# Kernel optimization log

Hardware: AMD Instinct MI355X
Metric: run time of the kernel (lower is better)

The kernel has to match this reference:

```python
import jax, jax.numpy as jnp
import numpy as np

B, S, D, H = 2, 2048, 1024, 16
DK = D // H  # 64


def rotate_half(x):
    d = x.shape[-1]
    x1, x2 = x[..., : d // 2], x[..., d // 2 :]
    return jnp.concatenate([-x2, x1], axis=-1)


def apply_rope(q, k):
    # q, k: [B, H, S, DK]
    d_k = q.shape[-1]
    seq_len = q.shape[-2]
    theta = 10000.0 ** (-2.0 / d_k * jnp.arange(d_k // 2, dtype=q.dtype))
    positions = jnp.arange(seq_len, dtype=q.dtype)
    angles = jnp.outer(positions, theta)                    # [S, DK/2]
    cos = jnp.tile(jnp.cos(angles), (1, 2))                 # [S, DK]
    sin = jnp.tile(jnp.sin(angles), (1, 2))
    q = q * cos + rotate_half(q) * sin
    k = k * cos + rotate_half(k) * sin
    return q, k


def setup_inputs() -> dict:
    key = jax.random.key(0)
    ks = jax.random.split(key, 9)
    std = 1.0 / np.sqrt(D)
    x = jax.random.normal(ks[0], (B, S, D), dtype=jnp.float32)
    # mask True = masked (code uses masked_fill(mask, -inf)); causal mask
    mask = jnp.triu(jnp.ones((S, S), dtype=bool), k=1)[None, None, :, :]
    mask = jnp.broadcast_to(mask, (B, 1, S, S))
    Wq = jax.random.uniform(ks[1], (D, D), jnp.float32, -std, std)
    bq = jax.random.uniform(ks[2], (D,), jnp.float32, -std, std)
    Wk = jax.random.uniform(ks[3], (D, D), jnp.float32, -std, std)
    bk = jax.random.uniform(ks[4], (D,), jnp.float32, -std, std)
    Wv = jax.random.uniform(ks[5], (D, D), jnp.float32, -std, std)
    bv = jax.random.uniform(ks[6], (D,), jnp.float32, -std, std)
    Wo = jax.random.uniform(ks[7], (D, D), jnp.float32, -std, std)
    bo = jax.random.uniform(ks[8], (D,), jnp.float32, -std, std)
    return {"x": x, "mask": mask, "Wq": Wq, "bq": bq, "Wk": Wk, "bk": bk,
            "Wv": Wv, "bv": bv, "Wo": Wo, "bo": bo}


def reference(x, mask, Wq, bq, Wk, bk, Wv, bv, Wo, bo):
    b, s, d = x.shape
    # projections -> [B, H, S, DK]
    q = (x @ Wq + bq).reshape(b, s, H, DK).transpose(0, 2, 1, 3)
    k = (x @ Wk + bk).reshape(b, s, H, DK).transpose(0, 2, 1, 3)
    v = (x @ Wv + bv).reshape(b, s, H, DK).transpose(0, 2, 1, 3)
    q, k = apply_rope(q, k)
    scores = jnp.einsum("bhqd,bhkd->bhqk", q, k) / np.sqrt(DK)
    scores = jnp.where(mask, -jnp.inf, scores)
    probs = jax.nn.softmax(scores, axis=-1)
    attn = jnp.einsum("bhqk,bhkd->bhqd", probs, v)
    o = attn.transpose(0, 2, 1, 3).reshape(b, s, H * DK)
    return o @ Wo + bo
```

## Files before the change

### kernel.cpp

```cpp
#include <hip/hip_runtime.h>
#include <hip/hip_bf16.h>
#include <math.h>

typedef __hip_bfloat16 bf16;
typedef __attribute__((ext_vector_type(8))) short short8;
typedef __attribute__((ext_vector_type(4))) short s16x4;
typedef __attribute__((ext_vector_type(4))) float f32x4;

#define B_  2
#define S_  2048
#define D_  1024
#define H_  16
#define DK_ 64

#define QSCALE 0.18033688011112043f
#define EXPOFF 11.541560327111707f

__device__ inline short bfs(float f) { return __builtin_bit_cast(short, __float2bfloat16(f)); }

#define GLL16(gptr, lptr)                                                        \
    __builtin_amdgcn_global_load_lds(                                            \
        (const __attribute__((address_space(1))) void*)(gptr),                   \
        (__attribute__((address_space(3))) void*)(lptr), 16, 0, 0)

#if __has_builtin(__builtin_amdgcn_mfma_f32_16x16x16bf16_1k)
#define MFMA_16x16x16(A, Bv, C) __builtin_amdgcn_mfma_f32_16x16x16bf16_1k(A, Bv, C, 0, 0, 0)
#elif __has_builtin(__builtin_amdgcn_mfma_f32_16x16x16_bf16)
#define MFMA_16x16x16(A, Bv, C) __builtin_amdgcn_mfma_f32_16x16x16_bf16(A, Bv, C, 0, 0, 0)
#else
static __device__ inline f32x4 mfma16_asm(s16x4 a, s16x4 b, f32x4 c) {
    f32x4 d;
    asm volatile("v_mfma_f32_16x16x16_bf16 %0, %1, %2, %3\n\ts_nop 7\n\ts_nop 7"
                 : "=v"(d) : "v"(a), "v"(b), "v"(c));
    return d;
}
#define MFMA_16x16x16(A, Bv, C) mfma16_asm(A, Bv, C)
#endif

__global__ __launch_bounds__(256)
void prep_k(const float* __restrict__ x,
            const float* __restrict__ W0, const float* __restrict__ W1,
            const float* __restrict__ W2, const float* __restrict__ W3,
            bf16* __restrict__ cx, bf16* __restrict__ Wt,
            float2* __restrict__ rope)
{
    const int z = blockIdx.z;
    const int t = threadIdx.x;
    if (z == 4) {
        const int bid = blockIdx.y * 16 + blockIdx.x;
        #pragma unroll
        for (int i = 0; i < 16; i++) {
            const size_t g = ((size_t)bid * 256 + t) * 4 + (size_t)i * 262144;
            const float4 v = *(const float4*)(x + g);
            s16x4 o = { bfs(v.x), bfs(v.y), bfs(v.z), bfs(v.w) };
            *(s16x4*)(cx + g) = o;
        }
        return;
    }
    if (z == 5) {
        const int bid = blockIdx.y * 16 + blockIdx.x;
        const int idx = bid * 256 + t;
        const int s = idx >> 5, dk = idx & 31;
        const float th = exp2f((float)dk * -0.41524101186092029f);
        float sn, cs;
        sincosf((float)s * th, &sn, &cs);
        rope[idx] = make_float2(cs, sn);
        return;
    }
    __shared__ float Lt[64][65];
    const float* W = (z == 0) ? W0 : (z == 1) ? W1 : (z == 2) ? W2 : W3;
    bf16* dst = Wt + (size_t)z * D_ * D_;
    const int k0 = blockIdx.y * 64, n0 = blockIdx.x * 64;
    #pragma unroll
    for (int p = 0; p < 4; p++) {
        const int idx = p * 256 + t;
        const int row = idx >> 4, cb = (idx & 15) * 4;
        const float4 v = *(const float4*)(W + (size_t)(k0 + row) * D_ + n0 + cb);
        Lt[cb + 0][row] = v.x; Lt[cb + 1][row] = v.y;
        Lt[cb + 2][row] = v.z; Lt[cb + 3][row] = v.w;
    }
    __syncthreads();
    #pragma unroll
    for (int p = 0; p < 4; p++) {
        const int idx = p * 256 + t;
        const int n = idx >> 4, kb = (idx & 15) * 4;
        s16x4 o = { bfs(Lt[n][kb]), bfs(Lt[n][kb + 1]), bfs(Lt[n][kb + 2]), bfs(Lt[n][kb + 3]) };
        *(s16x4*)(dst + (size_t)(n0 + n) * D_ + k0 + kb) = o;
    }
}

__global__ __launch_bounds__(256)
void gemm_qkv(const bf16* __restrict__ A, const bf16* __restrict__ WtAll,
              const float* __restrict__ b0, const float* __restrict__ b1,
              const float* __restrict__ b2, const float2* __restrict__ rope,
              bf16* __restrict__ d0, bf16* __restrict__ d1, bf16* __restrict__ d2)
{
    constexpr int K = D_;
    const int L = (int)blockIdx.x;
    const int m0 = (L & 31) * 128;
    const int rest = L >> 5;
    const int z = rest >> 4;
    const int n0 = (rest & 15) * 64;
    const bf16* W = WtAll + (size_t)z * D_ * D_;
    const float* bias = (z == 0) ? b0 : (z == 1) ? b1 : b2;

    __shared__ __align__(16) short As[128 * 64];
    __shared__ __align__(16) short Bs[64 * 64];

    const int t = threadIdx.x;
    const int wave = t >> 6, lane = t & 63, quad = lane >> 4, l16 = lane & 15;
    const int wm = wave * 32;

    const int srow  = t >> 3;
    const int sslot = (t & 7) ^ (srow & 7);
    const bf16* gA = A + (size_t)(m0 + srow) * K + sslot * 8;
    const bf16* gW = W + (size_t)(n0 + srow) * K + sslot * 8;
    const int wb = wave * 512;

    f32x4 acc[2][4] = {};

    for (int k0 = 0; k0 < K; k0 += 64) {
        __syncthreads();
        GLL16(gA + k0,                  &As[wb]);
        GLL16(gA + k0 + (size_t)32 * K, &As[2048 + wb]);
        GLL16(gA + k0 + (size_t)64 * K, &As[4096 + wb]);
        GLL16(gA + k0 + (size_t)96 * K, &As[6144 + wb]);
        GLL16(gW + k0,                  &Bs[wb]);
        GLL16(gW + k0 + (size_t)32 * K, &Bs[2048 + wb]);
        __syncthreads();

        const int swz = l16 & 7;
        #pragma unroll
        for (int c = 0; c < 2; c++) {
            const int slot = ((c * 4 + quad) ^ swz) * 8;
            short8 af[2], bfv[4];
            #pragma unroll
            for (int i = 0; i < 2; i++) af[i] = *(const short8*)&As[(wm + i * 16 + l16) * 64 + slot];
            #pragma unroll
            for (int j = 0; j < 4; j++) bfv[j] = *(const short8*)&Bs[(j * 16 + l16) * 64 + slot];
            #pragma unroll
            for (int i = 0; i < 2; i++)
                #pragma unroll
                for (int j = 0; j < 4; j++)
                    acc[i][j] = __builtin_amdgcn_mfma_f32_16x16x32_bf16(af[i], bfv[j], acc[i][j], 0, 0, 0);
        }
    }

    if (z == 2) {
        const int h = n0 >> 6;
        #pragma unroll
        for (int j = 0; j < 4; j++) {
            const int ncol = n0 + j * 16 + l16;
            const float bb = bias[ncol];
            const int dk = ncol & 63;
            #pragma unroll
            for (int i = 0; i < 2; i++) {
                const int mbase = m0 + wm + i * 16 + quad * 4;
                #pragma unroll
                for (int r = 0; r < 4; r++) {
                    const int m = mbase + r;
                    const int b = m >> 11, s = m & (S_ - 1);
                    d2[(((size_t)(b * H_ + h)) * DK_ + dk) * S_ + s] = __float2bfloat16(acc[i][j][r] + bb);
                }
            }
        }
    } else {
        bf16* dst = z ? d1 : d0;
        const float sc = z ? 1.0f : QSCALE;
        const int h = n0 >> 6;
        #pragma unroll
        for (int j = 0; j < 2; j++) {
            const int dk = j * 16 + l16;
            const float blo = bias[(h << 6) + dk];
            const float bhi = bias[(h << 6) + dk + 32];
            #pragma unroll
            for (int i = 0; i < 2; i++) {
                #pragma unroll
                for (int r = 0; r < 4; r++) {
                    const int m = m0 + wm + i * 16 + quad * 4 + r;
                    const int b = m >> 11, s = m & (S_ - 1);
                    const float2 cc = rope[(s << 5) + dk];
                    const float v1 = acc[i][j][r] + blo;
                    const float v2 = acc[i][j + 2][r] + bhi;
                    bf16* p = dst + (((size_t)(b * H_ + h)) * S_ + s) * DK_;
                    p[dk]      = __float2bfloat16((v1 * cc.x - v2 * cc.y) * sc);
                    p[dk + 32] = __float2bfloat16((v2 * cc.x + v1 * cc.y) * sc);
                }
            }
        }
    }
}

__global__ __launch_bounds__(256)
void gemm_o(const bf16* __restrict__ A, const bf16* __restrict__ Wt3,
            const float* __restrict__ bias, float* __restrict__ fout)
{
    constexpr int K = D_;
    const int L = (int)blockIdx.x;
    const int m0 = (L & 63) * 64;
    const int n0 = (L >> 6) * 64;

    __shared__ __align__(16) short As[64 * 64];
    __shared__ __align__(16) short Bs[64 * 64];

    const int t = threadIdx.x;
    const int wave = t >> 6, lane = t & 63, quad = lane >> 4, l16 = lane & 15;
    const int wm = wave * 16;

    const int srow  = t >> 3;
    const int sslot = (t & 7) ^ (srow & 7);
    const bf16* gA = A   + (size_t)(m0 + srow) * K + sslot * 8;
    const bf16* gW = Wt3 + (size_t)(n0 + srow) * K + sslot * 8;
    const int wb = wave * 512;

    f32x4 acc[4] = {};

    for (int k0 = 0; k0 < K; k0 += 64) {
        __syncthreads();
        GLL16(gA + k0,                  &As[wb]);
        GLL16(gA + k0 + (size_t)32 * K, &As[2048 + wb]);
        GLL16(gW + k0,                  &Bs[wb]);
        GLL16(gW + k0 + (size_t)32 * K, &Bs[2048 + wb]);
        __syncthreads();

        const int swz = l16 & 7;
        short8 af[2], bfv[4][2];
        #pragma unroll
        for (int c = 0; c < 2; c++) {
            af[c] = *(const short8*)&As[(wm + l16) * 64 + ((c * 4 + quad) ^ swz) * 8];
            #pragma unroll
            for (int j = 0; j < 4; j++)
                bfv[j][c] = *(const short8*)&Bs[(j * 16 + l16) * 64 + ((c * 4 + quad) ^ swz) * 8];
        }
        #pragma unroll
        for (int c = 0; c < 2; c++)
            #pragma unroll
            for (int j = 0; j < 4; j++)
                acc[j] = __builtin_amdgcn_mfma_f32_16x16x32_bf16(af[c], bfv[j][c], acc[j], 0, 0, 0);
    }

    #pragma unroll
    for (int j = 0; j < 4; j++) {
        const int ncol = n0 + j * 16 + l16;
        const float bb = bias[ncol];
        const int mbase = m0 + wm + quad * 4;
        #pragma unroll
        for (int r = 0; r < 4; r++)
            fout[(size_t)(mbase + r) * D_ + ncol] = acc[j][r] + bb;
    }
}

template<bool DIAG>
__device__ __forceinline__
void attn_tile(const short* __restrict__ Ks, const short* __restrict__ Vts,
               const short8 qf0, const short8 qf1,
               f32x4* ot, float& l_acc,
               const int wave, const int quad, const int l16)
{
    const int kkmax = DIAG ? wave : 3;
    #pragma unroll
    for (int kk = 0; kk <= kkmax; kk++) {
        const short8 kf0 = *(const short8*)&Ks[(kk * 16 + l16) * 72 + quad * 8];
        const short8 kf1 = *(const short8*)&Ks[(kk * 16 + l16) * 72 + 32 + quad * 8];
        f32x4 st = {};
        st = __builtin_amdgcn_mfma_f32_16x16x32_bf16(kf0, qf0, st, 0, 0, 0);
        st = __builtin_amdgcn_mfma_f32_16x16x32_bf16(kf1, qf1, st, 0, 0, 0);

        s16x4 pt;
        float psum = 0.0f;
        #pragma unroll
        for (int r = 0; r < 4; r++) {
            float p;
            if (DIAG) {
                const bool masked = (kk == wave) && (quad * 4 + r > l16);
                p = masked ? 0.0f : exp2f(st[r] - EXPOFF);
            } else {
                p = exp2f(st[r] - EXPOFF);
            }
            psum += p;
            pt[r] = bfs(p);
        }
        l_acc += psum;

        #pragma unroll
        for (int dt = 0; dt < 4; dt++) {
            const s16x4 vf = *(const s16x4*)&Vts[(dt * 16 + l16) * 72 + kk * 16 + quad * 4];
            ot[dt] = MFMA_16x16x16(vf, pt, ot[dt]);
        }
    }
}

__global__ __launch_bounds__(256)
void attn_k(const bf16* __restrict__ q_ws, const bf16* __restrict__ k_ws,
            const bf16* __restrict__ vt_ws, bf16* __restrict__ attn_ws)
{
    __shared__ __align__(16) short Ks[64 * 72];
    __shared__ __align__(16) short Vts[64 * 72];

    const int bh = (int)blockIdx.x;
    const int by = (int)blockIdx.y;
    const int j8 = by & 7, g = by >> 3;
    const int qt = (g == 0) ? (31 - j8) : (g == 1) ? j8 : (g == 2) ? (23 - j8) : (8 + j8);

    const int t = threadIdx.x;
    const int wave = t >> 6, quad = (t & 63) >> 4, l16 = t & 15;
    const bf16* Kb = k_ws + (size_t)bh * S_ * DK_;
    const bf16* Vb = vt_ws + (size_t)bh * DK_ * S_;
    const int b = bh >> 4, h = bh & 15;

    const bf16* Qb = q_ws + ((size_t)bh * S_ + qt * 64 + wave * 16) * DK_;
    const short8 qf0 = *(const short8*)(Qb + (size_t)l16 * DK_ + quad * 8);
    const short8 qf1 = *(const short8*)(Qb + (size_t)l16 * DK_ + 32 + quad * 8);

    float l_acc = 0.0f;
    f32x4 ot[4] = {};

    for (int kt = 0; kt <= qt; kt++) {
        __syncthreads();
        #pragma unroll
        for (int p = 0; p < 2; p++) {
            const int idx = p * 256 + t;
            const int row = idx >> 3, cb = (idx & 7) * 8;
            *(float4*)&Ks[row * 72 + cb]  = *(const float4*)(Kb + (size_t)(kt * 64 + row) * DK_ + cb);
            *(float4*)&Vts[row * 72 + cb] = *(const float4*)(Vb + (size_t)row * S_ + kt * 64 + cb);
        }
        __syncthreads();

        if (kt == qt) attn_tile<true >(Ks, Vts, qf0, qf1, ot, l_acc, wave, quad, l16);
        else          attn_tile<false>(Ks, Vts, qf0, qf1, ot, l_acc, wave, quad, l16);
    }

    l_acc += __shfl_xor(l_acc, 16, 64);
    l_acc += __shfl_xor(l_acc, 32, 64);
    const float inv = 1.0f / l_acc;
    const int srow = qt * 64 + wave * 16 + l16;
    bf16* orow = attn_ws + ((size_t)(b * S_ + srow)) * D_ + h * 64;
    #pragma unroll
    for (int dt = 0; dt < 4; dt++) {
        s16x4 o4 = { bfs(ot[dt][0] * inv), bfs(ot[dt][1] * inv),
                     bfs(ot[dt][2] * inv), bfs(ot[dt][3] * inv) };
        *(s16x4*)(orow + dt * 16 + quad * 4) = o4;
    }
}

extern "C" void kernel_launch(void* const* d_in, const int* in_sizes, int n_in,
                              void* d_out, int out_size, void* d_ws, size_t ws_size,
                              hipStream_t stream)
{
    (void)out_size; (void)ws_size;
    const float* x = nullptr;
    const float* W[4] = {nullptr, nullptr, nullptr, nullptr};
    const float* bias[4] = {nullptr, nullptr, nullptr, nullptr};
    int wi = 0, bi = 0;
    for (int i = 0; i < n_in; i++) {
        const int sz = in_sizes[i];
        if (sz == B_ * S_ * D_ && x == nullptr) x = (const float*)d_in[i];
        else if (sz == D_ * D_ && wi < 4) W[wi++] = (const float*)d_in[i];
        else if (sz == D_ && bi < 4) bias[bi++] = (const float*)d_in[i];
    }

    bf16* ws = (bf16*)d_ws;
    const size_t SEG = (size_t)B_ * S_ * D_;
    bf16* canonX  = ws;
    bf16* Wt      = ws + SEG;
    bf16* k_ws    = ws + 2 * SEG;
    bf16* vt_ws   = ws + 3 * SEG;
    bf16* attn_ws = canonX;
    bf16* q_ws    = (bf16*)d_out;
    float2* rope  = (float2*)((bf16*)d_out + SEG);

    prep_k<<<dim3(16, 16, 6), 256, 0, stream>>>(x, W[0], W[1], W[2], W[3], canonX, Wt, rope);

    gemm_qkv<<<dim3(1536, 1, 1), 256, 0, stream>>>(
        canonX, Wt, bias[0], bias[1], bias[2], rope, q_ws, k_ws, vt_ws);

    attn_k<<<dim3(32, 32), 256, 0, stream>>>(q_ws, k_ws, vt_ws, attn_ws);

    gemm_o<<<dim3(1024, 1, 1), 256, 0, stream>>>(
        attn_ws, Wt + (size_t)3 * D_ * D_, bias[3], (float*)d_out);
}
```

Before: 203.1 us.

## Process two query tiles per attention block to reuse K/V loads

Each attention block now handles two consecutive 64-row query tiles (128 rows), sharing each K/V tile loaded into LDS and the V fragments across both. The grid halves from 32x32 to 32x16 and the load-balancing query-tile mapping is adjusted. This is meant to halve global K/V traffic and LDS fill and sync overhead per query row. In exchange it doubles accumulator registers, which may lower occupancy, and leaves fewer blocks to spread the causal imbalance across CUs.

```diff
diff --git a/kernel.cpp b/kernel.cpp
--- a/kernel.cpp
+++ b/kernel.cpp
@@ -250,42 +250,67 @@
     }
 }
 
-template<bool DIAG>
+template<int MODE>
 __device__ __forceinline__
-void attn_tile(const short* __restrict__ Ks, const short* __restrict__ Vts,
-               const short8 qf0, const short8 qf1,
-               f32x4* ot, float& l_acc,
-               const int wave, const int quad, const int l16)
-{
-    const int kkmax = DIAG ? wave : 3;
+void attn_tile2(const short* __restrict__ Ks, const short* __restrict__ Vts,
+                const short8 qfA0, const short8 qfA1,
+                const short8 qfB0, const short8 qfB1,
+                f32x4* otA, float& lA, f32x4* otB, float& lB,
+                const int wave, const int quad, const int l16)
+{
+    const int kkmax = (MODE == 2) ? wave : 3;
     #pragma unroll
     for (int kk = 0; kk <= kkmax; kk++) {
         const short8 kf0 = *(const short8*)&Ks[(kk * 16 + l16) * 72 + quad * 8];
         const short8 kf1 = *(const short8*)&Ks[(kk * 16 + l16) * 72 + 32 + quad * 8];
-        f32x4 st = {};
-        st = __builtin_amdgcn_mfma_f32_16x16x32_bf16(kf0, qf0, st, 0, 0, 0);
-        st = __builtin_amdgcn_mfma_f32_16x16x32_bf16(kf1, qf1, st, 0, 0, 0);
-
-        s16x4 pt;
-        float psum = 0.0f;
-        #pragma unroll
-        for (int r = 0; r < 4; r++) {
-            float p;
-            if (DIAG) {
-                const bool masked = (kk == wave) && (quad * 4 + r > l16);
-                p = masked ? 0.0f : exp2f(st[r] - EXPOFF);
-            } else {
-                p = exp2f(st[r] - EXPOFF);
+        s16x4 vf[4];
+        #pragma unroll
+        for (int dt = 0; dt < 4; dt++)
+            vf[dt] = *(const s16x4*)&Vts[(dt * 16 + l16) * 72 + kk * 16 + quad * 4];
+
+        if (MODE == 0 || (MODE == 1 && kk <= wave)) {
+            f32x4 st = {};
+            st = __builtin_amdgcn_mfma_f32_16x16x32_bf16(kf0, qfA0, st, 0, 0, 0);
+            st = __builtin_amdgcn_mfma_f32_16x16x32_bf16(kf1, qfA1, st, 0, 0, 0);
+            s16x4 pt;
+            float ps = 0.0f;
+            #pragma unroll
+            for (int r = 0; r < 4; r++) {
+                float p;
+                if (MODE == 1) {
+                    const bool masked = (kk == wave) && (quad * 4 + r > l16);
+                    p = masked ? 0.0f : exp2f(st[r] - EXPOFF);
+                } else {
+                    p = exp2f(st[r] - EXPOFF);
+                }
+                ps += p;
+                pt[r] = bfs(p);
             }
-            psum += p;
-            pt[r] = bfs(p);
-        }
-        l_acc += psum;
-
-        #pragma unroll
-        for (int dt = 0; dt < 4; dt++) {
-            const s16x4 vf = *(const s16x4*)&Vts[(dt * 16 + l16) * 72 + kk * 16 + quad * 4];
-            ot[dt] = MFMA_16x16x16(vf, pt, ot[dt]);
+            lA += ps;
+            #pragma unroll
+            for (int dt = 0; dt < 4; dt++) otA[dt] = MFMA_16x16x16(vf[dt], pt, otA[dt]);
+        }
+        {
+            f32x4 st = {};
+            st = __builtin_amdgcn_mfma_f32_16x16x32_bf16(kf0, qfB0, st, 0, 0, 0);
+            st = __builtin_amdgcn_mfma_f32_16x16x32_bf16(kf1, qfB1, st, 0, 0, 0);
+            s16x4 pt;
+            float ps = 0.0f;
+            #pragma unroll
+            for (int r = 0; r < 4; r++) {
+                float p;
+                if (MODE == 2) {
+                    const bool masked = (kk == wave) && (quad * 4 + r > l16);
+                    p = masked ? 0.0f : exp2f(st[r] - EXPOFF);
+                } else {
+                    p = exp2f(st[r] - EXPOFF);
+                }
+                ps += p;
+                pt[r] = bfs(p);
+            }
+            lB += ps;
+            #pragma unroll
+            for (int dt = 0; dt < 4; dt++) otB[dt] = MFMA_16x16x16(vf[dt], pt, otB[dt]);
         }
     }
 }
@@ -300,7 +325,7 @@
     const int bh = (int)blockIdx.x;
     const int by = (int)blockIdx.y;
     const int j8 = by & 7, g = by >> 3;
-    const int qt = (g == 0) ? (31 - j8) : (g == 1) ? j8 : (g == 2) ? (23 - j8) : (8 + j8);
+    const int qt = (g == 0) ? (15 - j8) : j8;
 
     const int t = threadIdx.x;
     const int wave = t >> 6, quad = (t & 63) >> 4, l16 = t & 15;
@@ -308,14 +333,18 @@
     const bf16* Vb = vt_ws + (size_t)bh * DK_ * S_;
     const int b = bh >> 4, h = bh & 15;
 
-    const bf16* Qb = q_ws + ((size_t)bh * S_ + qt * 64 + wave * 16) * DK_;
-    const short8 qf0 = *(const short8*)(Qb + (size_t)l16 * DK_ + quad * 8);
-    const short8 qf1 = *(const short8*)(Qb + (size_t)l16 * DK_ + 32 + quad * 8);
-
-    float l_acc = 0.0f;
-    f32x4 ot[4] = {};
-
-    for (int kt = 0; kt <= qt; kt++) {
+    const int fa = 2 * qt, fb = 2 * qt + 1;
+    const bf16* QbA = q_ws + ((size_t)bh * S_ + qt * 128 + wave * 16) * DK_;
+    const bf16* QbB = QbA + (size_t)64 * DK_;
+    const short8 qfA0 = *(const short8*)(QbA + (size_t)l16 * DK_ + quad * 8);
+    const short8 qfA1 = *(const short8*)(QbA + (size_t)l16 * DK_ + 32 + quad * 8);
+    const short8 qfB0 = *(const short8*)(QbB + (size_t)l16 * DK_ + quad * 8);
+    const short8 qfB1 = *(const short8*)(QbB + (size_t)l16 * DK_ + 32 + quad * 8);
+
+    float lA = 0.0f, lB = 0.0f;
+    f32x4 otA[4] = {}, otB[4] = {};
+
+    for (int kt = 0; kt <= fb; kt++) {
         __syncthreads();
         #pragma unroll
         for (int p = 0; p < 2; p++) {
@@ -326,20 +355,27 @@
         }
         __syncthreads();
 
-        if (kt == qt) attn_tile<true >(Ks, Vts, qf0, qf1, ot, l_acc, wave, quad, l16);
-        else          attn_tile<false>(Ks, Vts, qf0, qf1, ot, l_acc, wave, quad, l16);
-    }
-
-    l_acc += __shfl_xor(l_acc, 16, 64);
-    l_acc += __shfl_xor(l_acc, 32, 64);
-    const float inv = 1.0f / l_acc;
-    const int srow = qt * 64 + wave * 16 + l16;
-    bf16* orow = attn_ws + ((size_t)(b * S_ + srow)) * D_ + h * 64;
+        if (kt < fa)       attn_tile2<0>(Ks, Vts, qfA0, qfA1, qfB0, qfB1, otA, lA, otB, lB, wave, quad, l16);
+        else if (kt == fa) attn_tile2<1>(Ks, Vts, qfA0, qfA1, qfB0, qfB1, otA, lA, otB, lB, wave, quad, l16);
+        else               attn_tile2<2>(Ks, Vts, qfA0, qfA1, qfB0, qfB1, otA, lA, otB, lB, wave, quad, l16);
+    }
+
+    lA += __shfl_xor(lA, 16, 64);
+    lA += __shfl_xor(lA, 32, 64);
+    lB += __shfl_xor(lB, 16, 64);
+    lB += __shfl_xor(lB, 32, 64);
+    const float invA = 1.0f / lA, invB = 1.0f / lB;
+    const int srowA = qt * 128 + wave * 16 + l16;
+    bf16* orowA = attn_ws + ((size_t)(b * S_ + srowA)) * D_ + h * 64;
+    bf16* orowB = orowA + (size_t)64 * D_;
     #pragma unroll
     for (int dt = 0; dt < 4; dt++) {
-        s16x4 o4 = { bfs(ot[dt][0] * inv), bfs(ot[dt][1] * inv),
-                     bfs(ot[dt][2] * inv), bfs(ot[dt][3] * inv) };
-        *(s16x4*)(orow + dt * 16 + quad * 4) = o4;
+        s16x4 oA = { bfs(otA[dt][0] * invA), bfs(otA[dt][1] * invA),
+                     bfs(otA[dt][2] * invA), bfs(otA[dt][3] * invA) };
+        s16x4 oB = { bfs(otB[dt][0] * invB), bfs(otB[dt][1] * invB),
+                     bfs(otB[dt][2] * invB), bfs(otB[dt][3] * invB) };
+        *(s16x4*)(orowA + dt * 16 + quad * 4) = oA;
+        *(s16x4*)(orowB + dt * 16 + quad * 4) = oB;
     }
 }
 
@@ -374,7 +410,7 @@
     gemm_qkv<<<dim3(1536, 1, 1), 256, 0, stream>>>(
         canonX, Wt, bias[0], bias[1], bias[2], rope, q_ws, k_ws, vt_ws);
 
-    attn_k<<<dim3(32, 32), 256, 0, stream>>>(q_ws, k_ws, vt_ws, attn_ws);
+    attn_k<<<dim3(32, 16), 256, 0, stream>>>(q_ws, k_ws, vt_ws, attn_ws);
 
     gemm_o<<<dim3(1024, 1, 1), 256, 0, stream>>>(
         attn_ws, Wt + (size_t)3 * D_ * D_, bias[3], (float*)d_out);
```

Result: slower. 210.5 us (+3.6%).
